# Kernel optimization log

Measured on AMD Instinct MI355X. Metric: run time of the kernel, lower is better.

## Reference

```python
import jax, jax.numpy as jnp
import numpy as np
from jax import lax

B, T_IN, E, T_OUT, N_MEL = 64, 512, 512, 800, 80
P, A_LSTM, D_LSTM, ATT, NF, K = 256, 1024, 1024, 128, 32, 31
PAD = (K - 1) // 2


def setup_inputs() -> dict:
    key = jax.random.key(0)
    ks = jax.random.split(key, 24)
    s = 0.02
    d = {}
    d['encoder_outputs'] = jax.random.normal(ks[0], (B, T_IN, E), jnp.float32)
    d['decoder_inputs'] = jax.random.normal(ks[1], (B, N_MEL, T_OUT), jnp.float32)
    d['text_lengths'] = jax.random.randint(ks[2], (B,), T_IN // 2, T_IN + 1)
    # prenet (two bias-free linears)
    d['Wp1'] = jax.random.normal(ks[3], (N_MEL, P), jnp.float32) * s
    d['Wp2'] = jax.random.normal(ks[4], (P, P), jnp.float32) * s
    # attention LSTMCell: input = prenet_dim + encoder_lstm_dim
    d['Wi_a'] = jax.random.normal(ks[5], (P + E, 4 * A_LSTM), jnp.float32) * s
    d['Wh_a'] = jax.random.normal(ks[6], (A_LSTM, 4 * A_LSTM), jnp.float32) * s
    d['b_a'] = jnp.zeros((4 * A_LSTM,), jnp.float32)
    # location-sensitive attention
    d['Wq'] = jax.random.normal(ks[7], (A_LSTM, ATT), jnp.float32) * s
    d['Wm'] = jax.random.normal(ks[8], (E, ATT), jnp.float32) * s
    d['Wv'] = jax.random.normal(ks[9], (ATT,), jnp.float32) * s
    d['Kloc'] = jax.random.normal(ks[10], (NF, 2, K), jnp.float32) * s   # OIH conv kernel
    d['Wloc'] = jax.random.normal(ks[11], (NF, ATT), jnp.float32) * s
    # decoder LSTMCell: input = attention_lstm_dim + encoder_lstm_dim
    d['Wi_d'] = jax.random.normal(ks[12], (A_LSTM + E, 4 * D_LSTM), jnp.float32) * s
    d['Wh_d'] = jax.random.normal(ks[13], (D_LSTM, 4 * D_LSTM), jnp.float32) * s
    d['b_d'] = jnp.zeros((4 * D_LSTM,), jnp.float32)
    # projections from [decoder_hidden ; attention_context]
    d['Wproj'] = jax.random.normal(ks[14], (D_LSTM + E, N_MEL), jnp.float32) * s
    d['bproj'] = jnp.zeros((N_MEL,), jnp.float32)
    d['Wgate'] = jax.random.normal(ks[15], (D_LSTM + E,), jnp.float32) * s
    d['bgate'] = jnp.zeros((), jnp.float32)
    return d


def _lstm_cell(x, h, c, Wi, Wh, b):
    g = x @ Wi + h @ Wh + b
    i, f, gg, o = jnp.split(g, 4, axis=-1)  # torch LSTMCell gate order i,f,g,o
    c = jax.nn.sigmoid(f) * c + jax.nn.sigmoid(i) * jnp.tanh(gg)
    h = jax.nn.sigmoid(o) * jnp.tanh(c)
    return h, c


def reference(encoder_outputs, decoder_inputs, text_lengths,
              Wp1, Wp2, Wi_a, Wh_a, b_a, Wq, Wm, Wv, Kloc, Wloc,
              Wi_d, Wh_d, b_d, Wproj, bproj, Wgate, bgate):
    b, t_in, e = encoder_outputs.shape
    t_out = decoder_inputs.shape[2]
    valid = jnp.arange(t_in)[None, :] < text_lengths[:, None]  # [B,T_in]
    pm = encoder_outputs @ Wm                                   # processed memory [B,T_in,ATT]

    # parse_decoder_inputs + go frame -> [T_out, B, n_mel] (n_frames_per_step=1)
    x = jnp.transpose(decoder_inputs, (2, 0, 1))
    x = jnp.concatenate([jnp.zeros((1, b, N_MEL), x.dtype), x], 0)[:t_out]
    # prenet over all steps (dropout disabled: eval-mode reference)
    h = jax.nn.relu(jax.nn.relu(x @ Wp1) @ Wp2)                 # [T_out,B,P]

    def step(carry, xt):
        ah, ac, dh, dc, aw, awc, ctx = carry
        ah, ac = _lstm_cell(jnp.concatenate([xt, ctx], -1), ah, ac, Wi_a, Wh_a, b_a)
        cat = jnp.stack([aw, awc], axis=1)                      # [B,2,T_in]
        loc = lax.conv_general_dilated(cat, Kloc, (1,), [(PAD, PAD)],
                                       dimension_numbers=('NCH', 'OIH', 'NCH'))  # [B,NF,T_in]
        ploc = jnp.einsum('bft,fa->bta', loc, Wloc)             # [B,T_in,ATT]
        energies = jnp.einsum('bta,a->bt',
                              jnp.tanh((ah @ Wq)[:, None, :] + ploc + pm), Wv)
        energies = jnp.where(valid, energies, -1e9)
        aw = jax.nn.softmax(energies, axis=1)                   # [B,T_in]
        ctx = jnp.einsum('bt,bte->be', aw, encoder_outputs)
        awc = awc + aw
        dh, dc = _lstm_cell(jnp.concatenate([ah, ctx], -1), dh, dc, Wi_d, Wh_d, b_d)
        hc = jnp.concatenate([dh, ctx], -1)
        mel = hc @ Wproj + bproj                                # [B,N_MEL]
        gate = hc @ Wgate + bgate                               # [B]
        return (ah, ac, dh, dc, aw, awc, ctx), (mel, gate, aw)

    z = lambda *s: jnp.zeros(s, encoder_outputs.dtype)
    init = (z(b, A_LSTM), z(b, A_LSTM), z(b, D_LSTM), z(b, D_LSTM),
            z(b, t_in), z(b, t_in), z(b, e))
    _, (mels, gates, aws) = lax.scan(step, init, h)
    mel_outputs = jnp.transpose(mels, (1, 2, 0))                # [B,N_MEL,T_out]
    gate_outputs = jnp.transpose(gates, (1, 0))                 # [B,T_out]
    alignments = jnp.transpose(aws, (1, 0, 2))                  # [B,T_out,T_in]
    return mel_outputs, gate_outputs, alignments
```

## Files before the change

kernel.cpp:

```cpp
#include <hip/hip_runtime.h>
#include <math.h>

#define NBLK 256
#define NTHR 512

#define BB    64
#define TIN   512
#define EEE   512
#define TOUTT 800
#define NMEL  80
#define PPP   256
#define ALS   1024
#define DLS   1024
#define ATTD  128
#define KA    1792
#define KD    2560

typedef _Float16 f16;
typedef f16 f16x8 __attribute__((ext_vector_type(8)));
typedef f16 f16x2 __attribute__((ext_vector_type(2)));
typedef float f32x4 __attribute__((ext_vector_type(4)));
typedef unsigned long long u64;

#define WTA_OFF   0ull
#define WTD_OFF   3670016ull
#define PM16_OFF  8912896ull
#define ENC16_OFF 11010048ull
#define PRE_OFF   19398656ull
#define XA_OFF    25952256ull
#define XD_OFF    26066944ull
#define AH16_OFF  26230784ull
#define DH16_OFF  26263552ull
#define CTX16_OFF 26296320ull
#define EN_OFF    26329088ull
#define WQT_OFF   26361856ull
#define WPJT_OFF  26427392ull
#define WP1T_OFF  26489600ull
#define WP2T_OFF  26499840ull
#define WLP_OFF   26532608ull
#define KLP_OFF   26534656ull
#define BAR_OFF   26535648ull

#define PL_O   0
#define RED_O  512
#define QL_O   528
#define PART_O 664

__device__ __forceinline__ float sigm(float x) { return 1.0f / (1.0f + __expf(-x)); }
__device__ __forceinline__ float ftanh(float x) {
  return 1.f - 2.f / (__expf(2.f * x) + 1.f);
}

union pk32 { unsigned u; f16x2 h; float f; };
__device__ __forceinline__ unsigned packh2(float a, float b) {
  pk32 p; p.h[0] = (f16)a; p.h[1] = (f16)b; return p.u;
}

__device__ __forceinline__ u64 ld64cg(const void* p) {
  return __hip_atomic_load((const u64*)p, __ATOMIC_RELAXED, __HIP_MEMORY_SCOPE_AGENT);
}
__device__ __forceinline__ void stu16cg(void* p, unsigned short v) {
  __hip_atomic_store((unsigned short*)p, v, __ATOMIC_RELAXED, __HIP_MEMORY_SCOPE_AGENT);
}
__device__ __forceinline__ void stu32cg(void* p, unsigned v) {
  __hip_atomic_store((unsigned*)p, v, __ATOMIC_RELAXED, __HIP_MEMORY_SCOPE_AGENT);
}
__device__ __forceinline__ f16x8 ld128cg(const f16* p) {
  union { u64 q[2]; f16x8 v; } r;
  r.q[0] = ld64cg(p);
  r.q[1] = ld64cg(p + 4);
  return r.v;
}

__device__ __forceinline__ size_t fragaddr(int b, int k) {
  return (size_t)(k >> 5) * 2048 + (size_t)(b >> 4) * 512 +
         (size_t)(((b & 15) + (((k & 31) >> 3) << 4)) << 3) + (k & 7);
}

__device__ __forceinline__ void gbar(unsigned* bar, unsigned& n, bool full) {
  n += 1;
  __syncthreads();
  if (threadIdx.x == 0) {
    if (full) __threadfence();
    __hip_atomic_fetch_add(&bar[(blockIdx.x & 15) << 4], 1u, __ATOMIC_RELAXED, __HIP_MEMORY_SCOPE_AGENT);
  }
  if (threadIdx.x < 64) {
    const unsigned tgt = n * 16u;
    const unsigned g = (threadIdx.x & 15) << 4;
    asm volatile("" ::: "memory");
    while (!__all((threadIdx.x >= 16) ||
                  (__hip_atomic_load(&bar[g], __ATOMIC_RELAXED, __HIP_MEMORY_SCOPE_AGENT) >= tgt)))
      __builtin_amdgcn_s_sleep(1);
    asm volatile("" ::: "memory");
    if (full) __threadfence();
  }
  __syncthreads();
}

__global__ void __launch_bounds__(256) transA(const float* __restrict__ Wi,
                                              const float* __restrict__ Wh,
                                              f16* __restrict__ Wt) {
  __shared__ float tile[64][65];
  const int tid = threadIdx.x;
  const int kb = (int)blockIdx.x % 28;
  const int cb = (int)blockIdx.x / 28;
  const int k0 = kb * 64, c0 = cb * 64;
  for (int i = tid; i < 4096; i += 256) {
    const int r = i >> 6, c = i & 63;
    const int k = k0 + r;
    const float v = (k < 768) ? Wi[(size_t)k * 4096 + c0 + c]
                              : Wh[(size_t)(k - 768) * 4096 + c0 + c];
    tile[c][r] = v;
  }
  __syncthreads();
  for (int i = tid; i < 4096; i += 256) {
    const int c = i >> 6, kk = i & 63;
    Wt[(size_t)(c0 + c) * KA + k0 + kk] = (f16)tile[c][kk];
  }
}

__global__ void __launch_bounds__(256) transD(const float* __restrict__ Wi,
                                              const float* __restrict__ Wh,
                                              f16* __restrict__ Wt) {
  __shared__ float tile[64][65];
  const int tid = threadIdx.x;
  const int kb = (int)blockIdx.x % 40;
  const int cb = (int)blockIdx.x / 40;
  const int k0 = kb * 64, c0 = cb * 64;
  for (int i = tid; i < 4096; i += 256) {
    const int r = i >> 6, c = i & 63;
    const int k = k0 + r;
    const float v = (k < 1536) ? Wi[(size_t)k * 4096 + c0 + c]
                               : Wh[(size_t)(k - 1536) * 4096 + c0 + c];
    tile[c][r] = v;
  }
  __syncthreads();
  for (int i = tid; i < 4096; i += 256) {
    const int c = i >> 6, kk = i & 63;
    Wt[(size_t)(c0 + c) * KD + k0 + kk] = (f16)tile[c][kk];
  }
}

__global__ void __launch_bounds__(128) pmk(const float* __restrict__ enc,
                                           const float* __restrict__ Wm,
                                           f16* __restrict__ pm16) {
  __shared__ float er[512];
  const int tid = threadIdx.x;
  const int b = (int)blockIdx.x >> 9, tt = (int)blockIdx.x & 511;
  for (int i = tid; i < 512; i += 128) er[i] = enc[((size_t)b * TIN + tt) * EEE + i];
  __syncthreads();
  float s = 0.f;
  #pragma unroll 4
  for (int k = 0; k < 512; ++k) s += er[k] * Wm[k * ATTD + tid];
  pm16[((size_t)b * TIN + tt) * ATTD + tid] = (f16)s;
}

__global__ void __launch_bounds__(512) enc16k(const float* __restrict__ enc,
                                              f16* __restrict__ e16) {
  const size_t i = ((size_t)blockIdx.x * 512 + threadIdx.x) * 8;
  const float4 v0 = *reinterpret_cast<const float4*>(enc + i);
  const float4 v1 = *reinterpret_cast<const float4*>(enc + i + 4);
  f16x8 o;
  o[0] = (f16)v0.x; o[1] = (f16)v0.y; o[2] = (f16)v0.z; o[3] = (f16)v0.w;
  o[4] = (f16)v1.x; o[5] = (f16)v1.y; o[6] = (f16)v1.z; o[7] = (f16)v1.w;
  *reinterpret_cast<f16x8*>(e16 + i) = o;
}

__global__ void __launch_bounds__(512) transAux(const float* __restrict__ Wq,
                                                const float* __restrict__ Wproj,
                                                const float* __restrict__ Wgate,
                                                const float* __restrict__ Wp1,
                                                const float* __restrict__ Wp2,
                                                const float* __restrict__ Wloc,
                                                const float* __restrict__ Kloc,
                                                f16* __restrict__ wqt,
                                                f16* __restrict__ wpjt,
                                                f16* __restrict__ wp1t,
                                                f16* __restrict__ wp2t,
                                                unsigned* __restrict__ wlocp,
                                                unsigned* __restrict__ klp) {
  const int idx = (int)blockIdx.x * 512 + (int)threadIdx.x;
  if (idx < 131072) {
    const int a = idx >> 10, k = idx & 1023;
    wqt[idx] = (f16)Wq[k * 128 + a];
  } else if (idx < 131072 + 124416) {
    const int j = idx - 131072;
    const int m = j / 1536, k = j % 1536;
    wpjt[j] = (f16)(m < 80 ? Wproj[k * 80 + m] : Wgate[k]);
  } else if (idx < 131072 + 124416 + 20480) {
    const int j = idx - (131072 + 124416);
    const int col = j / 80, k = j % 80;
    wp1t[j] = (f16)Wp1[k * 256 + col];
  } else if (idx < 131072 + 124416 + 20480 + 65536) {
    const int j = idx - (131072 + 124416 + 20480);
    const int col = j >> 8, k = j & 255;
    wp2t[j] = (f16)Wp2[k * 256 + col];
  } else if (idx < 131072 + 124416 + 20480 + 65536 + 2048) {
    const int j = idx - (131072 + 124416 + 20480 + 65536);
    const int a = j >> 4, fp = j & 15;
    wlocp[j] = packh2(Wloc[(2 * fp) * 128 + a], Wloc[(2 * fp + 1) * 128 + a]);
  } else if (idx < 131072 + 124416 + 20480 + 65536 + 2048 + 992) {
    const int j = idx - (131072 + 124416 + 20480 + 65536 + 2048);
    const int k = j >> 5, f = j & 31;
    klp[j] = packh2(Kloc[f * 62 + k], Kloc[f * 62 + 31 + k]);
  }
}

__global__ void __launch_bounds__(512) prenetk(const float* __restrict__ dec_in,
                                               const f16* __restrict__ wp1t,
                                               const f16* __restrict__ wp2t,
                                               f16* __restrict__ pre) {
  __shared__ float xl[64 * 80];
  __shared__ f16 h1l[64 * 264];
  const int t = (int)blockIdx.x;
  const int tid = threadIdx.x;
  f16* out = pre + (size_t)t * 16384;
  if (t == 0) {
    unsigned* o32 = (unsigned*)out;
    for (int i = tid; i < 8192; i += 512) o32[i] = 0u;
    return;
  }
  for (int i = tid; i < 5120; i += 512) {
    const int b = i / 80, m = i % 80;
    xl[b * 80 + m] = dec_in[(size_t)b * (NMEL * TOUTT) + (size_t)m * TOUTT + (t - 1)];
  }
  __syncthreads();
  {
    const int col = tid & 255, bh = tid >> 8;
    for (int bb = 0; bb < 32; ++bb) {
      const int b = bh * 32 + bb;
      float s = 0.f;
      #pragma unroll 4
      for (int k = 0; k < 80; ++k) s += xl[b * 80 + k] * (float)wp1t[col * 80 + k];
      h1l[b * 264 + col] = (f16)fmaxf(s, 0.f);
    }
  }
  __syncthreads();
  {
    const int col = tid & 255, bh = tid >> 8;
    for (int bb = 0; bb < 32; ++bb) {
      const int b = bh * 32 + bb;
      float s = 0.f;
      #pragma unroll 4
      for (int k = 0; k < 256; ++k) s += (float)h1l[b * 264 + k] * (float)wp2t[col * 256 + k];
      out[fragaddr(b, col)] = (f16)fmaxf(s, 0.f);
    }
  }
}

__device__ __forceinline__ void lstm_tail(int bid, int tid, float* smemf,
                                          const f32x4 c, int kh, int mt, int lane,
                                          const float* __restrict__ bias, float& creg,
                                          f16* __restrict__ h16,
                                          f16* frag1, int k1off,
                                          f16* frag2, int k2off) {
  float* Call = smemf;
  float* CallB = smemf + 1024;
  const int r0 = mt * 16 + (lane >> 4) * 4;
  const int n = lane & 15;
  if (kh == 1) {
    #pragma unroll
    for (int j = 0; j < 4; ++j) CallB[(r0 + j) * 16 + n] = c[j];
  }
  __syncthreads();
  if (kh == 0) {
    #pragma unroll
    for (int j = 0; j < 4; ++j) Call[(r0 + j) * 16 + n] = c[j] + CallB[(r0 + j) * 16 + n];
  }
  __syncthreads();
  if (tid < 256) {
    const int b = tid & 63, q = tid >> 6;
    const int cc = bid * 4 + q;
    const float g0 = Call[b * 16 + q]      + bias[cc];
    const float g1 = Call[b * 16 + 4 + q]  + bias[1024 + cc];
    const float g2 = Call[b * 16 + 8 + q]  + bias[2048 + cc];
    const float g3 = Call[b * 16 + 12 + q] + bias[3072 + cc];
    const float cn = sigm(g1) * creg + sigm(g0) * ftanh(g2);
    creg = cn;
    const float h = sigm(g3) * ftanh(cn);
    pk32 hp; hp.h[0] = (f16)h; hp.h[1] = (f16)0.f;
    const unsigned short hu = (unsigned short)(hp.u & 0xFFFFu);
    stu16cg(h16 + (size_t)b * 1024 + cc, hu);
    if (frag1) stu16cg(frag1 + fragaddr(b, k1off + cc), hu);
    if (frag2) stu16cg(frag2 + fragaddr(b, k2off + cc), hu);
  }
}

__device__ __forceinline__ void do_melgate(int b, int half, int tcol,
                                           const f16* __restrict__ dh16,
                                           const f16* __restrict__ ctx16p,
                                           const f16* __restrict__ wpjt,
                                           const float* __restrict__ bproj,
                                           const float* __restrict__ bgate,
                                           float* __restrict__ out_mel,
                                           float* __restrict__ out_gate,
                                           float* smem) {
  const int tid = threadIdx.x;
  __syncthreads();
  u64* dhl = (u64*)smem;
  u64* ctl = (u64*)smem + 256;
  if (tid < 256)      dhl[tid] = ld64cg((const u64*)(dh16 + (size_t)b * 1024) + tid);
  else if (tid < 384) ctl[tid - 256] = ld64cg((const u64*)(ctx16p + (size_t)b * 512) + (tid - 256));
  __syncthreads();
  float* melp = smem + 768;
  const int nrow = half ? 40 : 41;
  const int ml = tid / 12, kq = tid % 12;
  if (ml < nrow) {
    const int m = half * 41 + ml;
    const f16* wr = wpjt + (size_t)m * 1536 + kq * 128;
    const f16* xl = (kq < 8) ? ((const f16*)dhl + kq * 128)
                             : ((const f16*)ctl + (kq - 8) * 128);
    float s = 0.f;
    #pragma unroll
    for (int c8 = 0; c8 < 16; ++c8) {
      const f16x8 xv = *reinterpret_cast<const f16x8*>(xl + c8 * 8);
      const f16x8 wv = *reinterpret_cast<const f16x8*>(wr + c8 * 8);
      #pragma unroll
      for (int j = 0; j < 8; ++j) s += (float)xv[j] * (float)wv[j];
    }
    melp[ml * 12 + kq] = s;
  }
  __syncthreads();
  if (tid < nrow) {
    float s = 0.f;
    #pragma unroll
    for (int j = 0; j < 12; ++j) s += melp[tid * 12 + j];
    const int m = half * 41 + tid;
    if (m < 80) out_mel[(size_t)b * NMEL * TOUTT + (size_t)m * TOUTT + tcol] = s + bproj[m];
    else        out_gate[(size_t)b * TOUTT + tcol] = s + bgate[0];
  }
}

__global__ void __launch_bounds__(NTHR, 1)
decoder_loop(const int* __restrict__ tlen,
             const float* __restrict__ b_a, const float* __restrict__ b_d,
             const float* __restrict__ Wv,
             const float* __restrict__ bproj, const float* __restrict__ bgate,
             const f16* __restrict__ wta_h, const f16* __restrict__ wtd_h,
             const f16* __restrict__ pm16, const f16* __restrict__ enc16,
             const f16* __restrict__ pre_h,
             const f16* __restrict__ wqt, const f16* __restrict__ wpjt,
             const unsigned* __restrict__ wlocp, const unsigned* __restrict__ klp,
             f16* __restrict__ xa_h, f16* __restrict__ xd_h,
             f16* __restrict__ ah16, f16* __restrict__ dh16,
             f16* __restrict__ ctx16, float* __restrict__ en,
             unsigned* bar,
             float* __restrict__ out_mel, float* __restrict__ out_gate,
             float* __restrict__ out_align) {
  __shared__ f16 wfA[28672];
  __shared__ f16 wfD[40960];
  __shared__ float smem[2048];
  __shared__ unsigned awb[544];

  const int tid = threadIdx.x;
  const int bid = (int)blockIdx.x;
  const int lane = tid & 63;
  const int w = tid >> 6;
  const int mt = w & 3, kh = w >> 2;
  const int b = bid & 63;
  const int chn = bid >> 6;
  unsigned syncn = 0;
  (void)en;

  for (int i = tid; i < 3584; i += NTHR) {
    const int ks = i >> 6, l = i & 63;
    const int n = l & 15, kc = (l >> 4) * 8;
    const int gcol = (n >> 2) * 1024 + bid * 4 + (n & 3);
    const uint4 v = *reinterpret_cast<const uint4*>(wta_h + (size_t)gcol * KA + ks * 32 + kc);
    *reinterpret_cast<uint4*>(&wfA[(size_t)i * 8]) = v;
  }
  for (int i = tid; i < 5120; i += NTHR) {
    const int ks = i >> 6, l = i & 63;
    const int n = l & 15, kc = (l >> 4) * 8;
    const int gcol = (n >> 2) * 1024 + bid * 4 + (n & 3);
    const uint4 v = *reinterpret_cast<const uint4*>(wtd_h + (size_t)gcol * KD + ks * 32 + kc);
    *reinterpret_cast<uint4*>(&wfD[(size_t)i * 8]) = v;
  }
  for (int i = tid; i < 544; i += NTHR) awb[i] = 0u;
  {
    unsigned* za = (unsigned*)xa_h;
    const int gid = bid * NTHR + tid;
    for (int i = gid; i < 278528; i += NBLK * NTHR) za[i] = 0u;
  }
  gbar(bar, syncn, true);

  const int len = tlen[b];
  float awcf = 0.f;
  float cregA = 0.f, cregD = 0.f;

  for (int t = 0; t <= TOUTT; ++t) {
    if (t > 0) {
      const f16* xdP = xd_h + (size_t)((t - 1) & 1) * 163840;
      const f16* abase = xdP + (size_t)(kh * 40) * 2048 + mt * 512 + lane * 8;
      const f16* bbase = wfD + ((size_t)(kh * 40) * 64 + lane) * 8;
      f32x4 c = {0.f, 0.f, 0.f, 0.f};
      #pragma unroll 8
      for (int ks = 0; ks < 40; ++ks) {
        const f16x8 af = ld128cg(abase + (size_t)ks * 2048);
        const f16x8 bf = *reinterpret_cast<const f16x8*>(bbase + (size_t)ks * 512);
        c = __builtin_amdgcn_mfma_f32_16x16x32_f16(af, bf, c, 0, 0, 0);
      }
      lstm_tail(bid, tid, smem, c, kh, mt, lane, b_d, cregD, dh16,
                xd_h + (size_t)(t & 1) * 163840, 1536, (f16*)0, 0);
    }
    if (t < TOUTT) {
      const f16* xaP = xa_h + (size_t)(t & 1) * 114688;
      const f16* preP = pre_h + (size_t)t * 16384;
      const f16* bbase = wfA + ((size_t)(kh * 28) * 64 + lane) * 8;
      f32x4 c = {0.f, 0.f, 0.f, 0.f};
      #pragma unroll 8
      for (int ks = 0; ks < 28; ++ks) {
        const int kg = kh * 28 + ks;
        const f16* ap = (kg < 8) ? preP : xaP;
        const f16x8 af = (kg < 8)
            ? *reinterpret_cast<const f16x8*>(ap + (size_t)kg * 2048 + mt * 512 + lane * 8)
            : ld128cg(ap + (size_t)kg * 2048 + mt * 512 + lane * 8);
        const f16x8 bf = *reinterpret_cast<const f16x8*>(bbase + (size_t)ks * 512);
        c = __builtin_amdgcn_mfma_f32_16x16x32_f16(af, bf, c, 0, 0, 0);
      }
      lstm_tail(bid, tid, smem, c, kh, mt, lane, b_a, cregA, ah16,
                xa_h + (size_t)((t + 1) & 1) * 114688, 768,
                xd_h + (size_t)(t & 1) * 163840, 0);
    }
    gbar(bar, syncn, false);

    if (t == TOUTT) {
      if (chn == 1 || chn == 2)
        do_melgate(b, chn - 1, TOUTT - 1, dh16, ctx16 + (size_t)((TOUTT - 1) & 1) * 32768,
                   wpjt, bproj, bgate, out_mel, out_gate, smem);
      break;
    }

    {
      u64* ahl = (u64*)smem;
      if (tid < 256) ahl[tid] = ld64cg((const u64*)(ah16 + (size_t)b * 1024) + tid);
      __syncthreads();
      {
        const int a = tid & 127, kq = tid >> 7;
        const f16* arow = (const f16*)ahl + kq * 256;
        const f16* wr = wqt + (size_t)a * 1024 + kq * 256;
        float s = 0.f;
        #pragma unroll 8
        for (int c8 = 0; c8 < 32; ++c8) {
          const f16x8 xv = *reinterpret_cast<const f16x8*>(arow + c8 * 8);
          const f16x8 wv = *reinterpret_cast<const f16x8*>(wr + c8 * 8);
          #pragma unroll
          for (int j = 0; j < 8; ++j) s += (float)xv[j] * (float)wv[j];
        }
        smem[PART_O + kq * 128 + a] = s;
      }
      __syncthreads();
      if (tid < 128) {
        const int a = tid;
        smem[QL_O + a + (a >> 5)] = smem[PART_O + a] + smem[PART_O + 128 + a] +
                                    smem[PART_O + 256 + a] + smem[PART_O + 384 + a];
      }
      __syncthreads();

      const int tt = tid;
      float lf[32];
      #pragma unroll
      for (int f = 0; f < 32; ++f) lf[f] = 0.f;
      for (int k = 0; k < 31; ++k) {
        pk32 v; v.u = awb[1 + tt + k];
        #pragma unroll
        for (int f = 0; f < 32; ++f) {
          pk32 kv; kv.u = klp[k * 32 + f];
          lf[f] = __builtin_amdgcn_fdot2(v.h, kv.h, lf[f], false);
        }
      }
      pk32 l2[16];
      #pragma unroll
      for (int fp = 0; fp < 16; ++fp) l2[fp].u = packh2(lf[2 * fp], lf[2 * fp + 1]);

      float e = 0.f;
      {
        const f16* pmrow = pm16 + (size_t)(b * TIN + tt) * ATTD;
        #pragma unroll 2
        for (int ao = 0; ao < 16; ++ao) {
          const f16x8 pmv = *reinterpret_cast<const f16x8*>(pmrow + ao * 8);
          #pragma unroll
          for (int i = 0; i < 8; ++i) {
            const int a = ao * 8 + i;
            float pa = 0.f;
            #pragma unroll
            for (int fp = 0; fp < 16; ++fp) {
              pk32 wv; wv.u = wlocp[a * 16 + fp];
              pa = __builtin_amdgcn_fdot2(l2[fp].h, wv.h, pa, false);
            }
            e += Wv[a] * ftanh(smem[QL_O + a + (a >> 5)] + pa + (float)pmv[i]);
          }
        }
      }

      const float ee = (tt < len) ? e : -1e30f;
      float m = ee;
      #pragma unroll
      for (int o = 32; o > 0; o >>= 1) m = fmaxf(m, __shfl_xor(m, o));
      if (lane == 0) smem[RED_O + w] = m;
      __syncthreads();
      if (tid == 0) {
        float mm = smem[RED_O];
        #pragma unroll
        for (int i = 1; i < 8; ++i) mm = fmaxf(mm, smem[RED_O + i]);
        smem[RED_O + 8] = mm;
      }
      __syncthreads();
      const float M = smem[RED_O + 8];
      const float p = (tt < len) ? __expf(ee - M) : 0.f;
      float s = p;
      #pragma unroll
      for (int o = 32; o > 0; o >>= 1) s += __shfl_xor(s, o);
      if (lane == 0) smem[RED_O + w] = s;
      __syncthreads();
      if (tid == 0) {
        float ss = smem[RED_O];
        #pragma unroll
        for (int i = 1; i < 8; ++i) ss += smem[RED_O + i];
        smem[RED_O + 8] = ss;
      }
      __syncthreads();
      const float an = p * (1.f / smem[RED_O + 8]);
      smem[PL_O + tid] = an;
      awcf += an;
      awb[16 + tid] = packh2(an, awcf);
      if (chn == 0) out_align[((size_t)b * TOUTT + t) * TIN + tid] = an;
      __syncthreads();

      {
        const int eo = lane & 15, sub4 = lane >> 4;
        float a8[8];
        #pragma unroll
        for (int i = 0; i < 8; ++i) a8[i] = 0.f;
        const f16* ebase = enc16 + (size_t)(b * TIN) * EEE + chn * 128 + eo * 8;
        #pragma unroll 4
        for (int j = 0; j < 16; ++j) {
          const int tj = w * 64 + sub4 * 16 + j;
          const float wv = smem[PL_O + tj];
          const f16x8 ev = __builtin_nontemporal_load(
              reinterpret_cast<const f16x8*>(ebase + (size_t)tj * EEE));
          #pragma unroll
          for (int i = 0; i < 8; ++i) a8[i] += wv * (float)ev[i];
        }
        #pragma unroll
        for (int i = 0; i < 8; ++i) {
          a8[i] += __shfl_xor(a8[i], 16);
          a8[i] += __shfl_xor(a8[i], 32);
        }
        if (lane < 16) {
          #pragma unroll
          for (int i = 0; i < 8; ++i) smem[PART_O + w * 128 + eo * 8 + i] = a8[i];
        }
      }
      __syncthreads();
      if (tid < 128) {
        float v = 0.f;
        #pragma unroll
        for (int ww = 0; ww < 8; ++ww) v += smem[PART_O + ww * 128 + tid];
        smem[PL_O + tid] = v;
      }
      __syncthreads();
      if (tid < 64) {
        const int ecol = chn * 128 + 2 * tid;
        const unsigned pv = packh2(smem[PL_O + 2 * tid], smem[PL_O + 2 * tid + 1]);
        stu32cg((unsigned*)(xa_h + (size_t)((t + 1) & 1) * 114688 + fragaddr(b, 256 + ecol)), pv);
        stu32cg((unsigned*)(xd_h + (size_t)(t & 1) * 163840 + fragaddr(b, 1024 + ecol)), pv);
        stu32cg((unsigned*)(ctx16 + (size_t)(t & 1) * 32768 + (size_t)b * 512 + ecol), pv);
      }
      if (t > 0 && (chn == 1 || chn == 2))
        do_melgate(b, chn - 1, t - 1, dh16, ctx16 + (size_t)((t - 1) & 1) * 32768,
                   wpjt, bproj, bgate, out_mel, out_gate, smem);
    }
    gbar(bar, syncn, false);
  }
}

extern "C" void kernel_launch(void* const* d_in, const int* in_sizes, int n_in,
                              void* d_out, int out_size, void* d_ws, size_t ws_size,
                              hipStream_t stream) {
  (void)in_sizes; (void)n_in; (void)out_size; (void)ws_size;
  const float* enc    = (const float*)d_in[0];
  const float* dec_in = (const float*)d_in[1];
  const int*   tlen   = (const int*)d_in[2];
  const float* Wp1    = (const float*)d_in[3];
  const float* Wp2    = (const float*)d_in[4];
  const float* Wi_a   = (const float*)d_in[5];
  const float* Wh_a   = (const float*)d_in[6];
  const float* b_a    = (const float*)d_in[7];
  const float* Wq     = (const float*)d_in[8];
  const float* Wm     = (const float*)d_in[9];
  const float* Wv     = (const float*)d_in[10];
  const float* Kloc   = (const float*)d_in[11];
  const float* Wloc   = (const float*)d_in[12];
  const float* Wi_d   = (const float*)d_in[13];
  const float* Wh_d   = (const float*)d_in[14];
  const float* b_d    = (const float*)d_in[15];
  const float* Wproj  = (const float*)d_in[16];
  const float* bproj  = (const float*)d_in[17];
  const float* Wgate  = (const float*)d_in[18];
  const float* bgate  = (const float*)d_in[19];

  float* ws = (float*)d_ws;
  f16*   wta_h = (f16*)(ws + WTA_OFF);
  f16*   wtd_h = (f16*)(ws + WTD_OFF);
  f16*   pm16  = (f16*)(ws + PM16_OFF);
  f16*   e16   = (f16*)(ws + ENC16_OFF);
  f16*   pre_h = (f16*)(ws + PRE_OFF);
  f16*   xa_h  = (f16*)(ws + XA_OFF);
  f16*   xd_h  = (f16*)(ws + XD_OFF);
  f16*   ah16  = (f16*)(ws + AH16_OFF);
  f16*   dh16  = (f16*)(ws + DH16_OFF);
  f16*   ctx16 = (f16*)(ws + CTX16_OFF);
  float* en    = ws + EN_OFF;
  f16*   wqt   = (f16*)(ws + WQT_OFF);
  f16*   wpjt  = (f16*)(ws + WPJT_OFF);
  f16*   wp1t  = (f16*)(ws + WP1T_OFF);
  f16*   wp2t  = (f16*)(ws + WP2T_OFF);
  unsigned* wlocp = (unsigned*)(ws + WLP_OFF);
  unsigned* klp   = (unsigned*)(ws + KLP_OFF);
  unsigned* bar   = (unsigned*)(ws + BAR_OFF);

  float* out_mel   = (float*)d_out;
  float* out_gate  = out_mel + (size_t)BB * NMEL * TOUTT;
  float* out_align = out_gate + (size_t)BB * TOUTT;

  hipMemsetAsync(bar, 0, 272 * sizeof(unsigned), stream);
  transA<<<dim3(28 * 64), dim3(256), 0, stream>>>(Wi_a, Wh_a, wta_h);
  transD<<<dim3(40 * 64), dim3(256), 0, stream>>>(Wi_d, Wh_d, wtd_h);
  pmk<<<dim3(BB * TIN), dim3(128), 0, stream>>>(enc, Wm, pm16);
  enc16k<<<dim3(4096), dim3(512), 0, stream>>>(enc, e16);
  transAux<<<dim3(673), dim3(512), 0, stream>>>(Wq, Wproj, Wgate, Wp1, Wp2, Wloc, Kloc,
                                                wqt, wpjt, wp1t, wp2t, wlocp, klp);
  prenetk<<<dim3(TOUTT), dim3(512), 0, stream>>>(dec_in, wp1t, wp2t, pre_h);
  decoder_loop<<<dim3(NBLK), dim3(NTHR), 0, stream>>>(
      tlen, b_a, b_d, Wv, bproj, bgate,
      wta_h, wtd_h, pm16, e16, pre_h, wqt, wpjt, wlocp, klp,
      xa_h, xd_h, ah16, dh16, ctx16, en, bar,
      out_mel, out_gate, out_align);
}
```

Measured before the change: 56.82 ms.

## Fold location conv and Wloc into one matrix and compute with MFMA

Precomputes the product of the location conv kernel and the Wloc projection into a single fp16 weight matrix of 62 taps by 128 attention dims, packed in MFMA B-fragment layout by a new setup kernel. Inside the per-step attention, each wave now runs 16x16x32 MFMAs over rows of the packed previous/cumulative alignment window instead of per-thread scalar fdot2 loops through 32 filters. Energies are reduced across lanes with shuffles and staged in shared memory before the softmax. The gain relies on the algebraic fusion removing the intermediate 32-filter stage, with slightly different fp16 rounding and extra scattered pm16 loads per lane.

```diff
diff --git a/kernel.cpp b/kernel.cpp
--- a/kernel.cpp
+++ b/kernel.cpp
@@ -166,19 +166,32 @@
   *reinterpret_cast<f16x8*>(e16 + i) = o;
 }
 
+__global__ void __launch_bounds__(256) kwk(const float* __restrict__ Kloc,
+                                           const float* __restrict__ Wloc,
+                                           f16* __restrict__ kwb) {
+  const int idx = (int)blockIdx.x * 256 + (int)threadIdx.x;
+  const int kc = idx >> 7, a = idx & 127;
+  const int k = kc >> 1, cch = kc & 1;
+  float s = 0.f;
+  if (k < 31) {
+    #pragma unroll 8
+    for (int f = 0; f < 32; ++f)
+      s += Kloc[f * 62 + cch * 31 + k] * Wloc[f * 128 + a];
+  }
+  const int ct = a >> 4, n = a & 15;
+  const int ks = kc >> 5, kcl = kc & 31, kch = kcl >> 3, j = kcl & 7;
+  kwb[((size_t)(ct * 2 + ks) * 64 + (kch * 16 + n)) * 8 + j] = (f16)s;
+}
+
 __global__ void __launch_bounds__(512) transAux(const float* __restrict__ Wq,
                                                 const float* __restrict__ Wproj,
                                                 const float* __restrict__ Wgate,
                                                 const float* __restrict__ Wp1,
                                                 const float* __restrict__ Wp2,
-                                                const float* __restrict__ Wloc,
-                                                const float* __restrict__ Kloc,
                                                 f16* __restrict__ wqt,
                                                 f16* __restrict__ wpjt,
                                                 f16* __restrict__ wp1t,
-                                                f16* __restrict__ wp2t,
-                                                unsigned* __restrict__ wlocp,
-                                                unsigned* __restrict__ klp) {
+                                                f16* __restrict__ wp2t) {
   const int idx = (int)blockIdx.x * 512 + (int)threadIdx.x;
   if (idx < 131072) {
     const int a = idx >> 10, k = idx & 1023;
@@ -195,14 +208,6 @@
     const int j = idx - (131072 + 124416 + 20480);
     const int col = j >> 8, k = j & 255;
     wp2t[j] = (f16)Wp2[k * 256 + col];
-  } else if (idx < 131072 + 124416 + 20480 + 65536 + 2048) {
-    const int j = idx - (131072 + 124416 + 20480 + 65536);
-    const int a = j >> 4, fp = j & 15;
-    wlocp[j] = packh2(Wloc[(2 * fp) * 128 + a], Wloc[(2 * fp + 1) * 128 + a]);
-  } else if (idx < 131072 + 124416 + 20480 + 65536 + 2048 + 992) {
-    const int j = idx - (131072 + 124416 + 20480 + 65536 + 2048);
-    const int k = j >> 5, f = j & 31;
-    klp[j] = packh2(Kloc[f * 62 + k], Kloc[f * 62 + 31 + k]);
   }
 }
 
@@ -340,10 +345,10 @@
              const f16* __restrict__ pm16, const f16* __restrict__ enc16,
              const f16* __restrict__ pre_h,
              const f16* __restrict__ wqt, const f16* __restrict__ wpjt,
-             const unsigned* __restrict__ wlocp, const unsigned* __restrict__ klp,
+             const f16* __restrict__ kwb,
              f16* __restrict__ xa_h, f16* __restrict__ xd_h,
              f16* __restrict__ ah16, f16* __restrict__ dh16,
-             f16* __restrict__ ctx16, float* __restrict__ en,
+             f16* __restrict__ ctx16,
              unsigned* bar,
              float* __restrict__ out_mel, float* __restrict__ out_gate,
              float* __restrict__ out_align) {
@@ -360,7 +365,6 @@
   const int b = bid & 63;
   const int chn = bid >> 6;
   unsigned syncn = 0;
-  (void)en;
 
   for (int i = tid; i < 3584; i += NTHR) {
     const int ks = i >> 6, l = i & 63;
@@ -457,43 +461,59 @@
       }
       __syncthreads();
 
-      const int tt = tid;
-      float lf[32];
+      float qlv[8], wvv[8];
       #pragma unroll
-      for (int f = 0; f < 32; ++f) lf[f] = 0.f;
-      for (int k = 0; k < 31; ++k) {
-        pk32 v; v.u = awb[1 + tt + k];
-        #pragma unroll
-        for (int f = 0; f < 32; ++f) {
-          pk32 kv; kv.u = klp[k * 32 + f];
-          lf[f] = __builtin_amdgcn_fdot2(v.h, kv.h, lf[f], false);
-        }
-      }
-      pk32 l2[16];
-      #pragma unroll
-      for (int fp = 0; fp < 16; ++fp) l2[fp].u = packh2(lf[2 * fp], lf[2 * fp + 1]);
-
-      float e = 0.f;
-      {
-        const f16* pmrow = pm16 + (size_t)(b * TIN + tt) * ATTD;
-        #pragma unroll 2
-        for (int ao = 0; ao < 16; ++ao) {
-          const f16x8 pmv = *reinterpret_cast<const f16x8*>(pmrow + ao * 8);
+      for (int ct = 0; ct < 8; ++ct) {
+        const int a = ct * 16 + (lane & 15);
+        qlv[ct] = smem[QL_O + a + (a >> 5)];
+        wvv[ct] = Wv[a];
+      }
+
+      for (int rt4 = 0; rt4 < 4; ++rt4) {
+        const int rt = w * 4 + rt4;
+        const int r_a = rt * 16 + (lane & 15);
+        f32x4 c[8];
+        #pragma unroll
+        for (int ct = 0; ct < 8; ++ct) c[ct] = (f32x4){0.f, 0.f, 0.f, 0.f};
+        #pragma unroll
+        for (int ks = 0; ks < 2; ++ks) {
+          const int tap = (lane >> 4) * 4 + ks * 16;
+          union { unsigned u[4]; f16x8 v; } af;
           #pragma unroll
-          for (int i = 0; i < 8; ++i) {
-            const int a = ao * 8 + i;
-            float pa = 0.f;
-            #pragma unroll
-            for (int fp = 0; fp < 16; ++fp) {
-              pk32 wv; wv.u = wlocp[a * 16 + fp];
-              pa = __builtin_amdgcn_fdot2(l2[fp].h, wv.h, pa, false);
-            }
-            e += Wv[a] * ftanh(smem[QL_O + a + (a >> 5)] + pa + (float)pmv[i]);
+          for (int q4 = 0; q4 < 4; ++q4) af.u[q4] = awb[1 + r_a + tap + q4];
+          #pragma unroll
+          for (int ct = 0; ct < 8; ++ct) {
+            const f16x8 bf = *reinterpret_cast<const f16x8*>(
+                kwb + ((size_t)(ct * 2 + ks) * 64 + lane) * 8);
+            c[ct] = __builtin_amdgcn_mfma_f32_16x16x32_f16(af.v, bf, c[ct], 0, 0, 0);
           }
         }
-      }
-
-      const float ee = (tt < len) ? e : -1e30f;
+        float ep[4] = {0.f, 0.f, 0.f, 0.f};
+        #pragma unroll
+        for (int ct = 0; ct < 8; ++ct) {
+          const int a = ct * 16 + (lane & 15);
+          #pragma unroll
+          for (int j = 0; j < 4; ++j) {
+            const int r = rt * 16 + ((lane >> 4) << 2) + j;
+            const float pmv = (float)pm16[(size_t)(b * TIN + r) * ATTD + a];
+            ep[j] += wvv[ct] * ftanh(qlv[ct] + c[ct][j] + pmv);
+          }
+        }
+        #pragma unroll
+        for (int j = 0; j < 4; ++j) {
+          ep[j] += __shfl_xor(ep[j], 1);
+          ep[j] += __shfl_xor(ep[j], 2);
+          ep[j] += __shfl_xor(ep[j], 4);
+          ep[j] += __shfl_xor(ep[j], 8);
+        }
+        if ((lane & 15) == 0) {
+          #pragma unroll
+          for (int j = 0; j < 4; ++j)
+            smem[PL_O + rt * 16 + ((lane >> 4) << 2) + j] = ep[j];
+        }
+      }
+
+      const float ee = (tid < len) ? smem[PL_O + tid] : -1e30f;
       float m = ee;
       #pragma unroll
       for (int o = 32; o > 0; o >>= 1) m = fmaxf(m, __shfl_xor(m, o));
@@ -507,7 +527,7 @@
       }
       __syncthreads();
       const float M = smem[RED_O + 8];
-      const float p = (tt < len) ? __expf(ee - M) : 0.f;
+      const float p = (tid < len) ? __expf(ee - M) : 0.f;
       float s = p;
       #pragma unroll
       for (int o = 32; o > 0; o >>= 1) s += __shfl_xor(s, o);
@@ -611,14 +631,12 @@
   f16*   ah16  = (f16*)(ws + AH16_OFF);
   f16*   dh16  = (f16*)(ws + DH16_OFF);
   f16*   ctx16 = (f16*)(ws + CTX16_OFF);
-  float* en    = ws + EN_OFF;
+  f16*   kwb   = (f16*)(ws + EN_OFF);
   f16*   wqt   = (f16*)(ws + WQT_OFF);
   f16*   wpjt  = (f16*)(ws + WPJT_OFF);
   f16*   wp1t  = (f16*)(ws + WP1T_OFF);
   f16*   wp2t  = (f16*)(ws + WP2T_OFF);
-  unsigned* wlocp = (unsigned*)(ws + WLP_OFF);
-  unsigned* klp   = (unsigned*)(ws + KLP_OFF);
-  unsigned* bar   = (unsigned*)(ws + BAR_OFF);
+  unsigned* bar = (unsigned*)(ws + BAR_OFF);
 
   float* out_mel   = (float*)d_out;
   float* out_gate  = out_mel + (size_t)BB * NMEL * TOUTT;
@@ -629,12 +647,13 @@
   transD<<<dim3(40 * 64), dim3(256), 0, stream>>>(Wi_d, Wh_d, wtd_h);
   pmk<<<dim3(BB * TIN), dim3(128), 0, stream>>>(enc, Wm, pm16);
   enc16k<<<dim3(4096), dim3(512), 0, stream>>>(enc, e16);
-  transAux<<<dim3(673), dim3(512), 0, stream>>>(Wq, Wproj, Wgate, Wp1, Wp2, Wloc, Kloc,
-                                                wqt, wpjt, wp1t, wp2t, wlocp, klp);
+  kwk<<<dim3(32), dim3(256), 0, stream>>>(Kloc, Wloc, kwb);
+  transAux<<<dim3(667), dim3(512), 0, stream>>>(Wq, Wproj, Wgate, Wp1, Wp2,
+                                                wqt, wpjt, wp1t, wp2t);
   prenetk<<<dim3(TOUTT), dim3(512), 0, stream>>>(dec_in, wp1t, wp2t, pre_h);
   decoder_loop<<<dim3(NBLK), dim3(NTHR), 0, stream>>>(
       tlen, b_a, b_d, Wv, bproj, bgate,
-      wta_h, wtd_h, pm16, e16, pre_h, wqt, wpjt, wlocp, klp,
-      xa_h, xd_h, ah16, dh16, ctx16, en, bar,
+      wta_h, wtd_h, pm16, e16, pre_h, wqt, wpjt, kwb,
+      xa_h, xd_h, ah16, dh16, ctx16, bar,
       out_mel, out_gate, out_align);
 }
```

New measurement: 62.01 ms. 1.09x slower.
